# Optimization experiments

Hardware: AMD Instinct MI355X
Metric: run time of the kernel (lower is better)

The kernel has to match this reference:

```python
import jax, jax.numpy as jnp
import numpy as np
from jax import lax

N = 100000   # input points
M = 100000   # output points
CIN = 64
COUT = 64
K = 3        # cubic kernel size
G = 50       # grid side (points live at voxel centers of a G^3 grid)
SHIFT = 1    # coordinate shift so border queries (coord -1) stay non-negative
B = 64       # per-axis encode base, > G + K; key fits easily in int32


def _encode(c):
    # c: [..., 3] int32 xyz voxel coords -> unique int32 key
    c = c + SHIFT
    return (c[..., 2] * B + c[..., 1]) * B + c[..., 0]


def setup_inputs() -> dict:
    rng = np.random.RandomState(0)
    total = G ** 3

    def decode(idx):
        x = idx % G
        y = (idx // G) % G
        z = idx // (G * G)
        # +0.5 moves points to voxel centers (as in the layer's docstring example)
        return np.stack([x, y, z], axis=1).astype(np.float32) + 0.5

    inp_positions = jnp.asarray(decode(rng.permutation(total)[:N]))
    out_positions = jnp.asarray(decode(rng.permutation(total)[:M]))

    key = jax.random.key(0)
    k1, k2 = jax.random.split(key, 2)
    inp_features = jax.random.normal(k1, (N, CIN), jnp.float32)
    kernel = jax.random.normal(k2, (K, K, K, CIN, COUT), jnp.float32) * 0.05
    bias = jnp.zeros((COUT,), jnp.float32)
    voxel_size = jnp.ones((), jnp.float32)
    return {
        "inp_features": inp_features,
        "inp_positions": inp_positions,
        "out_positions": out_positions,
        "voxel_size": voxel_size,
        "kernel": kernel,
        "bias": bias,
    }


def reference(inp_features, inp_positions, out_positions, voxel_size, kernel, bias):
    # SparseConv on a regular grid: odd cubic kernel -> offset = 0, Linf radius
    # K*voxel*0.51 selects exactly the K^3 voxel neighborhood. Nearest-neighbor
    # interpolation with identity mapping maps relative offset d in [-r, r]^3
    # to filter tap index d + r on each axis (x = width = last spatial dim).
    inp_coord = jnp.floor(inp_positions / voxel_size).astype(jnp.int32)  # [N,3]
    out_coord = jnp.floor(out_positions / voxel_size).astype(jnp.int32)  # [M,3]

    # sorted-key hash table over input voxels
    keys = _encode(inp_coord)                    # [N]
    order = jnp.argsort(keys)
    skeys = keys[order]
    feats = inp_features[order]                  # [N, Cin]

    r = K // 2
    K3 = K ** 3
    ks = jnp.arange(K3)
    # flat kernel order is (z, y, x) to match kernel.reshape(K3, Cin, Cout)
    d_xyz = jnp.stack([ks % K - r, (ks // K) % K - r, ks // (K * K) - r],
                      axis=1).astype(jnp.int32)  # [K3, 3]
    Kmat = kernel.reshape(K3, CIN, COUT)

    n_inp = skeys.shape[0]

    def step(acc, xs):
        d, W = xs                                 # d: [3], W: [Cin, Cout]
        qk = _encode(out_coord + d)               # [M]
        p = jnp.searchsorted(skeys, qk)
        pc = jnp.clip(p, 0, n_inp - 1)
        found = (skeys[pc] == qk)[:, None]        # [M, 1]
        g = jnp.where(found, feats[pc], 0.0)      # [M, Cin]
        return acc + g @ W, None

    out0 = jnp.zeros((out_coord.shape[0], COUT), inp_features.dtype)
    out, _ = lax.scan(step, out0, (d_xyz, Kmat))
    return out + bias
```

## Files before the change

### kernel.cpp

```cpp
#include <hip/hip_runtime.h>
#include <math.h>

#define GY 54
#define GZ 54
#define NROWS (54*54*64)

#define BXV 8
#define BYV 4
#define BZV 4
#define HX 10
#define HY 6
#define HZ 6
#define NH (HX*HY*HZ)
#define NBX 7
#define NBY 13
#define NBZ 13
#define NBRICK (NBX*NBY*NBZ)
#define SLAB 148

#define LDK 72

typedef __bf16  bf16x8 __attribute__((ext_vector_type(8)));
typedef float  f32x16 __attribute__((ext_vector_type(16)));

__global__ void scatter_feats_kernel(const float* __restrict__ feats,
                                     const float* __restrict__ pos,
                                     const float* __restrict__ vsp,
                                     __bf16* __restrict__ featsG, int n) {
    int t = blockIdx.x * 256 + threadIdx.x;
    int i = t >> 2, c = t & 3;
    if (i >= n) return;
    float vs = vsp[0];
    int x = (int)floorf(pos[3*i+0] / vs) + 1;
    int y = (int)floorf(pos[3*i+1] / vs) + 1;
    int z = (int)floorf(pos[3*i+2] / vs) + 1;
    int key = (z * GY + y) * 64 + x;
    const float4* src = (const float4*)(feats + (size_t)i * 64 + c * 16);
    float4 f0 = src[0], f1 = src[1], f2 = src[2], f3 = src[3];
    bf16x8 c0, c1;
    c0[0]=(__bf16)f0.x; c0[1]=(__bf16)f0.y; c0[2]=(__bf16)f0.z; c0[3]=(__bf16)f0.w;
    c0[4]=(__bf16)f1.x; c0[5]=(__bf16)f1.y; c0[6]=(__bf16)f1.z; c0[7]=(__bf16)f1.w;
    c1[0]=(__bf16)f2.x; c1[1]=(__bf16)f2.y; c1[2]=(__bf16)f2.z; c1[3]=(__bf16)f2.w;
    c1[4]=(__bf16)f3.x; c1[5]=(__bf16)f3.y; c1[6]=(__bf16)f3.z; c1[7]=(__bf16)f3.w;
    bf16x8* dst = (bf16x8*)(featsG + (size_t)key * 64 + c * 16);
    dst[0] = c0; dst[1] = c1;
}

__global__ void scatter_omap_kernel(const float* __restrict__ pos, int m,
                                    const float* __restrict__ vsp,
                                    int* __restrict__ omap) {
    int i = blockIdx.x * 256 + threadIdx.x;
    if (i >= m) return;
    float vs = vsp[0];
    int x = (int)floorf(pos[3*i+0] / vs) + 1;
    int y = (int)floorf(pos[3*i+1] / vs) + 1;
    int z = (int)floorf(pos[3*i+2] / vs) + 1;
    omap[(z * GY + y) * 64 + x] = i;
}

__global__ void convw_kernel(const float* __restrict__ W, __bf16* __restrict__ Wt) {
    int i = blockIdx.x * 256 + threadIdx.x;
    if (i >= 27*64*64) return;
    int t  = i >> 12;
    int r  = i & 4095;
    int ci = r >> 6;
    int co = r & 63;
    Wt[(t << 12) + (co << 6) + ci] = (__bf16)W[i];
}

__global__ __launch_bounds__(256) void conv_kernel(
    const __bf16* __restrict__ featsG,
    const __bf16* __restrict__ Wt,
    const float* __restrict__ bias,
    const int*   __restrict__ omap,
    float*       __restrict__ out)
{
    __shared__ __align__(16) __bf16 halo[NH * LDK];
    __shared__ __align__(16) __bf16 Bld[64 * LDK];
    __shared__ int obuf[128];

    const int tid = threadIdx.x;

    int q = (blockIdx.x & 7) * SLAB + (blockIdx.x >> 3);
    if (q >= NBRICK) return;
    const int bx = q % NBX;
    int rem = q / NBX;
    const int by = rem % NBY;
    const int bz = rem / NBY;

    #pragma unroll
    for (int it = 0; it < 12; ++it) {
        int task = it * 256 + tid;
        if (task < NH * 8) {
            int r = task >> 3, c = task & 7;
            int xs = r % HX;
            int t2 = r / HX;
            int ys = t2 % HY;
            int zs = t2 / HY;
            int gkey = ((bz*BZV + zs) * GY + (by*BYV + ys)) * 64 + (bx*BXV + xs);
            *(float4*)(halo + r * LDK + c * 8) =
                *(const float4*)(featsG + (size_t)gkey * 64 + c * 8);
        }
    }
    if (tid < 128) {
        int x = tid & 7, y = (tid >> 3) & 3, z = tid >> 5;
        int key = ((bz*BZV + z + 1) * GY + (by*BYV + y + 1)) * 64 + (bx*BXV + x + 1);
        obuf[tid] = omap[key];
    }

    const int wave  = tid >> 6;
    const int lane  = tid & 63;
    const int lrow  = lane & 31;
    const int halfk = lane >> 5;
    const int xv = lrow & 7, yv = (lrow >> 3) & 3, zv = wave;
    const int r0 = (zv + 1) * (HX*HY) + (yv + 1) * HX + (xv + 1);
    const int Abase = r0 * LDK + halfk * 8;
    const int Bb0 = lrow * LDK + halfk * 8;
    const int Bb1 = (32 + lrow) * LDK + halfk * 8;

    const int wr0 = tid >> 3,        wc0 = tid & 7;
    const int wr1 = (256 + tid) >> 3, wc1 = tid & 7;

    float4 wreg0 = *(const float4*)(Wt + (size_t)wr0 * 64 + wc0 * 8);
    float4 wreg1 = *(const float4*)(Wt + (size_t)wr1 * 64 + wc1 * 8);

    f32x16 acc0, acc1;
    #pragma unroll
    for (int i = 0; i < 16; ++i) { acc0[i] = 0.f; acc1[i] = 0.f; }

    for (int t = 0; t < 27; ++t) {
        *(float4*)(Bld + wr0 * LDK + wc0 * 8) = wreg0;
        *(float4*)(Bld + wr1 * LDK + wc1 * 8) = wreg1;
        __syncthreads();

        if (t < 26) {
            const __bf16* wp = Wt + ((size_t)(t + 1) << 12);
            wreg0 = *(const float4*)(wp + wr0 * 64 + wc0 * 8);
            wreg1 = *(const float4*)(wp + wr1 * 64 + wc1 * 8);
        }

        const int dx = t % 3 - 1;
        const int dy = (t / 3) % 3 - 1;
        const int dz = t / 9 - 1;
        const __bf16* Ab = halo + Abase + (dz * (HX*HY) + dy * HX + dx) * LDK;

        #pragma unroll
        for (int kc = 0; kc < 4; ++kc) {
            bf16x8 a  = *(const bf16x8*)(Ab + kc * 16);
            bf16x8 b0 = *(const bf16x8*)(Bld + Bb0 + kc * 16);
            bf16x8 b1 = *(const bf16x8*)(Bld + Bb1 + kc * 16);
            acc0 = __builtin_amdgcn_mfma_f32_32x32x16_bf16(a, b0, acc0, 0, 0, 0);
            acc1 = __builtin_amdgcn_mfma_f32_32x32x16_bf16(a, b1, acc1, 0, 0, 0);
        }
        __syncthreads();
    }

    const int col0 = lrow, col1 = 32 + lrow;
    const float bv0 = bias[col0], bv1 = bias[col1];
    #pragma unroll
    for (int r = 0; r < 16; ++r) {
        int row = (r & 3) + 8 * (r >> 2) + 4 * halfk;
        int orow = obuf[wave * 32 + row];
        if (orow >= 0) {
            out[(size_t)orow * 64 + col0] = acc0[r] + bv0;
            out[(size_t)orow * 64 + col1] = acc1[r] + bv1;
        }
    }
}

extern "C" void kernel_launch(void* const* d_in, const int* in_sizes, int n_in,
                              void* d_out, int out_size, void* d_ws, size_t ws_size,
                              hipStream_t stream) {
    const float* feats = (const float*)d_in[0];
    const float* ipos  = (const float*)d_in[1];
    const float* opos  = (const float*)d_in[2];
    const float* vsp   = (const float*)d_in[3];
    const float* W     = (const float*)d_in[4];
    const float* bias  = (const float*)d_in[5];

    int N = in_sizes[0] / 64;
    int M = out_size / 64;

    __bf16* featsG = (__bf16*)d_ws;
    int*    omap   = (int*)((char*)d_ws + (size_t)NROWS * 128);
    __bf16* Wt     = (__bf16*)((char*)omap + (size_t)NROWS * 4);

    hipMemsetAsync(featsG, 0, (size_t)NROWS * 128, stream);
    hipMemsetAsync(omap, 0xFF, (size_t)NROWS * 4, stream);
    scatter_feats_kernel<<<(N*4 + 255) / 256, 256, 0, stream>>>(feats, ipos, vsp, featsG, N);
    scatter_omap_kernel<<<(M + 255) / 256, 256, 0, stream>>>(opos, M, vsp, omap);
    convw_kernel<<<(27*64*64 + 255) / 256, 256, 0, stream>>>(W, Wt);
    conv_kernel<<<8 * SLAB, 256, 0, stream>>>(featsG, Wt, bias, omap, (float*)d_out);
}
```

Measured before the change: 157.9 us.

## Replace dense bf16 feature grid with index map and gather in conv halo load

Drops the dense bf16 feature grid and its large memset. The prep step now scatters only an int index map for input voxels, and the three prep kernels are merged into one launch. The conv kernel gathers fp32 features through the index map and converts them to bf16 while loading the halo. Weights are read straight from global/L2 into registers instead of being staged through LDS, which removes the two per-tap barriers; occupancy is raised with a launch bounds hint. The cost is an indirect, uncoalesced halo gather, and every wave now re-fetches the weights from cache.

```diff
diff --git a/kernel.cpp b/kernel.cpp
--- a/kernel.cpp
+++ b/kernel.cpp
@@ -2,20 +2,14 @@
 #include <math.h>
 
 #define GY 54
-#define GZ 54
 #define NROWS (54*54*64)
 
-#define BXV 8
-#define BYV 4
-#define BZV 4
 #define HX 10
 #define HY 6
-#define HZ 6
-#define NH (HX*HY*HZ)
+#define NH 360
 #define NBX 7
 #define NBY 13
-#define NBZ 13
-#define NBRICK (NBX*NBY*NBZ)
+#define NBRICK (7*13*13)
 #define SLAB 148
 
 #define LDK 72
@@ -23,60 +17,44 @@
 typedef __bf16  bf16x8 __attribute__((ext_vector_type(8)));
 typedef float  f32x16 __attribute__((ext_vector_type(16)));
 
-__global__ void scatter_feats_kernel(const float* __restrict__ feats,
-                                     const float* __restrict__ pos,
-                                     const float* __restrict__ vsp,
-                                     __bf16* __restrict__ featsG, int n) {
-    int t = blockIdx.x * 256 + threadIdx.x;
-    int i = t >> 2, c = t & 3;
-    if (i >= n) return;
+__global__ void prep_kernel(const float* __restrict__ ipos, int n,
+                            const float* __restrict__ opos, int m,
+                            const float* __restrict__ vsp,
+                            const float* __restrict__ W,
+                            int* __restrict__ imap, int* __restrict__ omap,
+                            __bf16* __restrict__ Wt) {
+    int i = blockIdx.x * 256 + threadIdx.x;
     float vs = vsp[0];
-    int x = (int)floorf(pos[3*i+0] / vs) + 1;
-    int y = (int)floorf(pos[3*i+1] / vs) + 1;
-    int z = (int)floorf(pos[3*i+2] / vs) + 1;
-    int key = (z * GY + y) * 64 + x;
-    const float4* src = (const float4*)(feats + (size_t)i * 64 + c * 16);
-    float4 f0 = src[0], f1 = src[1], f2 = src[2], f3 = src[3];
-    bf16x8 c0, c1;
-    c0[0]=(__bf16)f0.x; c0[1]=(__bf16)f0.y; c0[2]=(__bf16)f0.z; c0[3]=(__bf16)f0.w;
-    c0[4]=(__bf16)f1.x; c0[5]=(__bf16)f1.y; c0[6]=(__bf16)f1.z; c0[7]=(__bf16)f1.w;
-    c1[0]=(__bf16)f2.x; c1[1]=(__bf16)f2.y; c1[2]=(__bf16)f2.z; c1[3]=(__bf16)f2.w;
-    c1[4]=(__bf16)f3.x; c1[5]=(__bf16)f3.y; c1[6]=(__bf16)f3.z; c1[7]=(__bf16)f3.w;
-    bf16x8* dst = (bf16x8*)(featsG + (size_t)key * 64 + c * 16);
-    dst[0] = c0; dst[1] = c1;
+    if (i < n) {
+        int x = (int)floorf(ipos[3*i+0] / vs) + 1;
+        int y = (int)floorf(ipos[3*i+1] / vs) + 1;
+        int z = (int)floorf(ipos[3*i+2] / vs) + 1;
+        imap[(z * GY + y) * 64 + x] = i;
+    } else if (i < n + m) {
+        int j = i - n;
+        int x = (int)floorf(opos[3*j+0] / vs) + 1;
+        int y = (int)floorf(opos[3*j+1] / vs) + 1;
+        int z = (int)floorf(opos[3*j+2] / vs) + 1;
+        omap[(z * GY + y) * 64 + x] = j;
+    } else if (i < n + m + 27*64*64) {
+        int k  = i - n - m;
+        int t  = k >> 12;
+        int r  = k & 4095;
+        int ci = r >> 6;
+        int co = r & 63;
+        Wt[(t << 12) + (co << 6) + ci] = (__bf16)W[k];
+    }
 }
 
-__global__ void scatter_omap_kernel(const float* __restrict__ pos, int m,
-                                    const float* __restrict__ vsp,
-                                    int* __restrict__ omap) {
-    int i = blockIdx.x * 256 + threadIdx.x;
-    if (i >= m) return;
-    float vs = vsp[0];
-    int x = (int)floorf(pos[3*i+0] / vs) + 1;
-    int y = (int)floorf(pos[3*i+1] / vs) + 1;
-    int z = (int)floorf(pos[3*i+2] / vs) + 1;
-    omap[(z * GY + y) * 64 + x] = i;
-}
-
-__global__ void convw_kernel(const float* __restrict__ W, __bf16* __restrict__ Wt) {
-    int i = blockIdx.x * 256 + threadIdx.x;
-    if (i >= 27*64*64) return;
-    int t  = i >> 12;
-    int r  = i & 4095;
-    int ci = r >> 6;
-    int co = r & 63;
-    Wt[(t << 12) + (co << 6) + ci] = (__bf16)W[i];
-}
-
-__global__ __launch_bounds__(256) void conv_kernel(
-    const __bf16* __restrict__ featsG,
+__global__ __launch_bounds__(256, 3) void conv_kernel(
+    const float* __restrict__ feats,
     const __bf16* __restrict__ Wt,
     const float* __restrict__ bias,
+    const int*   __restrict__ imap,
     const int*   __restrict__ omap,
     float*       __restrict__ out)
 {
     __shared__ __align__(16) __bf16 halo[NH * LDK];
-    __shared__ __align__(16) __bf16 Bld[64 * LDK];
     __shared__ int obuf[128];
 
     const int tid = threadIdx.x;
@@ -97,14 +75,24 @@
             int t2 = r / HX;
             int ys = t2 % HY;
             int zs = t2 / HY;
-            int gkey = ((bz*BZV + zs) * GY + (by*BYV + ys)) * 64 + (bx*BXV + xs);
-            *(float4*)(halo + r * LDK + c * 8) =
-                *(const float4*)(featsG + (size_t)gkey * 64 + c * 8);
+            int key = ((bz*4 + zs) * GY + (by*4 + ys)) * 64 + (bx*8 + xs);
+            int idx = imap[key];
+            bf16x8 v;
+            if (idx >= 0) {
+                const float4* s = (const float4*)(feats + (size_t)idx * 64 + c * 8);
+                float4 f0 = s[0], f1 = s[1];
+                v[0]=(__bf16)f0.x; v[1]=(__bf16)f0.y; v[2]=(__bf16)f0.z; v[3]=(__bf16)f0.w;
+                v[4]=(__bf16)f1.x; v[5]=(__bf16)f1.y; v[6]=(__bf16)f1.z; v[7]=(__bf16)f1.w;
+            } else {
+                #pragma unroll
+                for (int j = 0; j < 8; ++j) v[j] = (__bf16)0.f;
+            }
+            *(bf16x8*)(halo + r * LDK + c * 8) = v;
         }
     }
     if (tid < 128) {
         int x = tid & 7, y = (tid >> 3) & 3, z = tid >> 5;
-        int key = ((bz*BZV + z + 1) * GY + (by*BYV + y + 1)) * 64 + (bx*BXV + x + 1);
+        int key = ((bz*4 + z + 1) * GY + (by*4 + y + 1)) * 64 + (bx*8 + x + 1);
         obuf[tid] = omap[key];
     }
 
@@ -112,47 +100,47 @@
     const int lane  = tid & 63;
     const int lrow  = lane & 31;
     const int halfk = lane >> 5;
-    const int xv = lrow & 7, yv = (lrow >> 3) & 3, zv = wave;
-    const int r0 = (zv + 1) * (HX*HY) + (yv + 1) * HX + (xv + 1);
-    const int Abase = r0 * LDK + halfk * 8;
-    const int Bb0 = lrow * LDK + halfk * 8;
-    const int Bb1 = (32 + lrow) * LDK + halfk * 8;
-
-    const int wr0 = tid >> 3,        wc0 = tid & 7;
-    const int wr1 = (256 + tid) >> 3, wc1 = tid & 7;
-
-    float4 wreg0 = *(const float4*)(Wt + (size_t)wr0 * 64 + wc0 * 8);
-    float4 wreg1 = *(const float4*)(Wt + (size_t)wr1 * 64 + wc1 * 8);
+    const int xv = lrow & 7, yv = (lrow >> 3) & 3;
+    const int r0 = (wave + 1) * (HX*HY) + (yv + 1) * HX + (xv + 1);
+    const __bf16* Abase = halo + r0 * LDK + halfk * 8;
+    const __bf16* Wlane = Wt + (size_t)lrow * 64 + halfk * 8;
 
     f32x16 acc0, acc1;
     #pragma unroll
     for (int i = 0; i < 16; ++i) { acc0[i] = 0.f; acc1[i] = 0.f; }
 
+    __syncthreads();
+
+    #pragma unroll 1
     for (int t = 0; t < 27; ++t) {
-        *(float4*)(Bld + wr0 * LDK + wc0 * 8) = wreg0;
-        *(float4*)(Bld + wr1 * LDK + wc1 * 8) = wreg1;
-        __syncthreads();
-
-        if (t < 26) {
-            const __bf16* wp = Wt + ((size_t)(t + 1) << 12);
-            wreg0 = *(const float4*)(wp + wr0 * 64 + wc0 * 8);
-            wreg1 = *(const float4*)(wp + wr1 * 64 + wc1 * 8);
-        }
-
         const int dx = t % 3 - 1;
         const int dy = (t / 3) % 3 - 1;
         const int dz = t / 9 - 1;
-        const __bf16* Ab = halo + Abase + (dz * (HX*HY) + dy * HX + dx) * LDK;
+        const __bf16* Ab = Abase + (dz * (HX*HY) + dy * HX + dx) * LDK;
+        const __bf16* Wb = Wlane + ((size_t)t << 12);
 
-        #pragma unroll
-        for (int kc = 0; kc < 4; ++kc) {
-            bf16x8 a  = *(const bf16x8*)(Ab + kc * 16);
-            bf16x8 b0 = *(const bf16x8*)(Bld + Bb0 + kc * 16);
-            bf16x8 b1 = *(const bf16x8*)(Bld + Bb1 + kc * 16);
-            acc0 = __builtin_amdgcn_mfma_f32_32x32x16_bf16(a, b0, acc0, 0, 0, 0);
-            acc1 = __builtin_amdgcn_mfma_f32_32x32x16_bf16(a, b1, acc1, 0, 0, 0);
-        }
-        __syncthreads();
+        bf16x8 b0_0 = *(const bf16x8*)(Wb + 0*16);
+        bf16x8 b0_1 = *(const bf16x8*)(Wb + 1*16);
+        bf16x8 b0_2 = *(const bf16x8*)(Wb + 2*16);
+        bf16x8 b0_3 = *(const bf16x8*)(Wb + 3*16);
+        bf16x8 b1_0 = *(const bf16x8*)(Wb + 2048 + 0*16);
+        bf16x8 b1_1 = *(const bf16x8*)(Wb + 2048 + 1*16);
+        bf16x8 b1_2 = *(const bf16x8*)(Wb + 2048 + 2*16);
+        bf16x8 b1_3 = *(const bf16x8*)(Wb + 2048 + 3*16);
+
+        bf16x8 a0 = *(const bf16x8*)(Ab + 0*16);
+        bf16x8 a1 = *(const bf16x8*)(Ab + 1*16);
+        bf16x8 a2 = *(const bf16x8*)(Ab + 2*16);
+        bf16x8 a3 = *(const bf16x8*)(Ab + 3*16);
+
+        acc0 = __builtin_amdgcn_mfma_f32_32x32x16_bf16(a0, b0_0, acc0, 0, 0, 0);
+        acc1 = __builtin_amdgcn_mfma_f32_32x32x16_bf16(a0, b1_0, acc1, 0, 0, 0);
+        acc0 = __builtin_amdgcn_mfma_f32_32x32x16_bf16(a1, b0_1, acc0, 0, 0, 0);
+        acc1 = __builtin_amdgcn_mfma_f32_32x32x16_bf16(a1, b1_1, acc1, 0, 0, 0);
+        acc0 = __builtin_amdgcn_mfma_f32_32x32x16_bf16(a2, b0_2, acc0, 0, 0, 0);
+        acc1 = __builtin_amdgcn_mfma_f32_32x32x16_bf16(a2, b1_2, acc1, 0, 0, 0);
+        acc0 = __builtin_amdgcn_mfma_f32_32x32x16_bf16(a3, b0_3, acc0, 0, 0, 0);
+        acc1 = __builtin_amdgcn_mfma_f32_32x32x16_bf16(a3, b1_3, acc1, 0, 0, 0);
     }
 
     const int col0 = lrow, col1 = 32 + lrow;
@@ -181,14 +169,13 @@
     int N = in_sizes[0] / 64;
     int M = out_size / 64;
 
-    __bf16* featsG = (__bf16*)d_ws;
-    int*    omap   = (int*)((char*)d_ws + (size_t)NROWS * 128);
-    __bf16* Wt     = (__bf16*)((char*)omap + (size_t)NROWS * 4);
+    int*    imap = (int*)d_ws;
+    int*    omap = imap + NROWS;
+    __bf16* Wt   = (__bf16*)(omap + NROWS);
 
-    hipMemsetAsync(featsG, 0, (size_t)NROWS * 128, stream);
-    hipMemsetAsync(omap, 0xFF, (size_t)NROWS * 4, stream);
-    scatter_feats_kernel<<<(N*4 + 255) / 256, 256, 0, stream>>>(feats, ipos, vsp, featsG, N);
-    scatter_omap_kernel<<<(M + 255) / 256, 256, 0, stream>>>(opos, M, vsp, omap);
-    convw_kernel<<<(27*64*64 + 255) / 256, 256, 0, stream>>>(W, Wt);
-    conv_kernel<<<8 * SLAB, 256, 0, stream>>>(featsG, Wt, bias, omap, (float*)d_out);
+    hipMemsetAsync(imap, 0xFF, (size_t)2 * NROWS * sizeof(int), stream);
+    int total = N + M + 27*64*64;
+    prep_kernel<<<(total + 255) / 256, 256, 0, stream>>>(ipos, N, opos, M, vsp, W,
+                                                         imap, omap, Wt);
+    conv_kernel<<<8 * SLAB, 256, 0, stream>>>(feats, Wt, bias, imap, omap, (float*)d_out);
 }
```

New measurement: 246.6 us. 56.1% more time.
